# Kernel tuning notes

Measured on AMD Instinct MI355X. Metric: run time of the kernel, lower is better.

## Reference

```python
import jax, jax.numpy as jnp
import numpy as np

# Dimensions derived from Mamba.__init__: d_model=512 -> joint_latent=32, mamb_latent=D=640
NL, D, DIN, DS, DTR, DC = 4, 640, 1280, 16, 40, 4  # n_layer, d_model, d_inner, d_state, dt_rank, d_conv
B, V = 64, 30  # batch, joint-sequence length (repeat_joint_num)


def _rms(x, w, eps=1e-5):
    return x * jax.lax.rsqrt(jnp.mean(x * x, axis=-1, keepdims=True) + eps) * w


def _mamba_block(x, in_w, conv_w, conv_b, xp_w, dt_w, dt_b, A_log, D_skip, out_w):
    # x: [B, V, D]
    u, res = jnp.split(jnp.einsum('bvd,ed->bve', x, in_w), 2, axis=-1)  # each [B,V,DIN]
    # causal depthwise conv1d over V
    xc = jnp.pad(u.transpose(0, 2, 1), ((0, 0), (0, 0), (DC - 1, 0)))  # [B,DIN,V+DC-1]
    xc = jax.lax.conv_general_dilated(xc, conv_w[:, None, :], (1,), 'VALID',
                                      feature_group_count=DIN,
                                      dimension_numbers=('NCH', 'OIH', 'NCH'))
    u = jax.nn.silu(xc.transpose(0, 2, 1) + conv_b)  # [B,V,DIN]
    # input-dependent SSM params
    dbl = jnp.einsum('bvd,ed->bve', u, xp_w)  # [B,V,DTR+2*DS]
    delta, Bm, Cm = jnp.split(dbl, [DTR, DTR + DS], axis=-1)
    delta = jax.nn.softplus(jnp.einsum('bvr,dr->bvd', delta, dt_w) + dt_b)  # [B,V,DIN]
    A = -jnp.exp(A_log)  # [DIN,DS]
    dA = jnp.exp(delta[..., None] * A)                              # [B,V,DIN,DS]
    dBu = delta[..., None] * Bm[:, :, None, :] * u[..., None]       # [B,V,DIN,DS]

    def step(h, t):
        dA_t, dBu_t, C_t = t
        h = dA_t * h + dBu_t                      # [B,DIN,DS]
        return h, jnp.einsum('bds,bs->bd', h, C_t)

    h0 = jnp.zeros((x.shape[0], DIN, DS), x.dtype)
    _, ys = jax.lax.scan(step, h0, (dA.transpose(1, 0, 2, 3),
                                    dBu.transpose(1, 0, 2, 3),
                                    Cm.transpose(1, 0, 2)))
    y = ys.transpose(1, 0, 2) + u * D_skip        # [B,V,DIN]
    return jnp.einsum('bvd,ed->bve', y * jax.nn.silu(res), out_w)


def setup_inputs() -> dict:
    key = jax.random.key(0)
    ks = jax.random.split(key, 10)
    s = 0.02
    return {
        'x': jax.random.normal(ks[0], (B, V, D), jnp.float32),
        'vs': jax.random.randint(ks[1], (B,), 0, V),
        'norm_w': jnp.ones((NL, D), jnp.float32),
        'in_proj_w': s * jax.random.normal(ks[2], (NL, 2 * DIN, D), jnp.float32),
        'conv_w': s * jax.random.normal(ks[3], (NL, DIN, DC), jnp.float32),
        'conv_b': jnp.zeros((NL, DIN), jnp.float32),
        'x_proj_w': s * jax.random.normal(ks[4], (NL, DTR + 2 * DS, DIN), jnp.float32),
        'dt_proj_w': s * jax.random.normal(ks[5], (NL, DIN, DTR), jnp.float32),
        'dt_proj_b': jnp.full((NL, DIN), -4.0, jnp.float32) + 0.1 * jax.random.normal(ks[6], (NL, DIN), jnp.float32),
        'A_log': jnp.tile(jnp.log(jnp.arange(1.0, DS + 1.0, dtype=jnp.float32)), (NL, DIN, 1)),
        'D_skip': jnp.ones((NL, DIN), jnp.float32),
        'out_proj_w': s * jax.random.normal(ks[7], (NL, D, DIN), jnp.float32),
        'norm_f_w': jnp.ones((D,), jnp.float32),
    }


def reference(x, vs, norm_w, in_proj_w, conv_w, conv_b, x_proj_w, dt_proj_w,
              dt_proj_b, A_log, D_skip, out_proj_w, norm_f_w):
    bidx = jnp.arange(x.shape[0])[:, None]
    # batch-wise circular permutation over V (circular_permute_v)
    fwd_idx = (jnp.arange(V)[None, :] + V - vs[:, None]) % V  # [B,V]
    h = x[bidx, fwd_idx]
    for i in range(NL):
        h = h + _mamba_block(_rms(h, norm_w[i]), in_proj_w[i], conv_w[i], conv_b[i],
                             x_proj_w[i], dt_proj_w[i], dt_proj_b[i], A_log[i],
                             D_skip[i], out_proj_w[i])
    h = _rms(h, norm_f_w)
    # reverse_circular_permute_v
    rev_idx = (jnp.arange(V)[None, :] + vs[:, None]) % V
    return h[bidx, rev_idx]
```

## Files before the change

### kernel.cpp

```cpp
#include <hip/hip_runtime.h>
#include <math.h>

#define NLAYER 4
#define DMODEL 640
#define DINNER 1280
#define DSTATE 16
#define DTRANK 40
#define DCONV  4
#define BATCH  64
#define SEQ    30
#define MTOK   (BATCH*SEQ)
#define NPROJ  (2*DINNER)
#define NDBL   (DTRANK+2*DSTATE)
#define NDBLP  80
#define KSEGS  8
#define KSEG   (DINNER/KSEGS)
#define DTKP   64

#define Q1 (NLAYER*NPROJ*DMODEL/4)
#define Q2 (NLAYER*DMODEL*DINNER/4)
#define Q3 (NLAYER*NDBLP*DINNER/4)
#define Q4 (NLAYER*DINNER*DTKP/4)
#define WCTOT (Q1+Q2+Q3+Q4)

typedef unsigned short u16;
typedef __bf16 bf16x8 __attribute__((ext_vector_type(8)));
typedef float  f32x4  __attribute__((ext_vector_type(4)));
typedef unsigned short u16x8 __attribute__((ext_vector_type(8)));

__device__ __forceinline__ float siluf(float x) {
    return x / (1.0f + __expf(-x));
}

__device__ __forceinline__ u16 f2bf(float f) {
    unsigned int u = __float_as_uint(f);
    u += 0x7fffu + ((u >> 16) & 1u);
    return (u16)(u >> 16);
}

__device__ __forceinline__ float bf2f(u16 b) {
    return __uint_as_float(((unsigned int)b) << 16);
}

__global__ void k_permute(const float* __restrict__ x, const int* __restrict__ vs,
                          float* __restrict__ h) {
    int idx = blockIdx.x * blockDim.x + threadIdx.x;
    if (idx >= MTOK * DMODEL) return;
    int d  = idx % DMODEL;
    int mv = idx / DMODEL;
    int v  = mv % SEQ;
    int b  = mv / SEQ;
    int src = (v + SEQ - vs[b]) % SEQ;
    h[idx] = x[(b * SEQ + src) * DMODEL + d];
}

__global__ __launch_bounds__(256)
void k_wconv(const float* __restrict__ in_w, const float* __restrict__ out_w,
             const float* __restrict__ xp_w, const float* __restrict__ dt_w,
             u16* __restrict__ wbi, u16* __restrict__ wbo,
             u16* __restrict__ wbx, u16* __restrict__ wdt) {
    int i = blockIdx.x * 256 + threadIdx.x;
    if (i < Q1) {
        int j = i * 4;
        float4 v = *(const float4*)(in_w + j);
        ushort4 o;
        o.x = f2bf(v.x); o.y = f2bf(v.y); o.z = f2bf(v.z); o.w = f2bf(v.w);
        *(ushort4*)(wbi + j) = o;
    } else if (i < Q1 + Q2) {
        int j = (i - Q1) * 4;
        float4 v = *(const float4*)(out_w + j);
        ushort4 o;
        o.x = f2bf(v.x); o.y = f2bf(v.y); o.z = f2bf(v.z); o.w = f2bf(v.w);
        *(ushort4*)(wbo + j) = o;
    } else if (i < Q1 + Q2 + Q3) {
        int j = (i - Q1 - Q2) * 4;
        int layer = j / (NDBLP * DINNER);
        int rem   = j % (NDBLP * DINNER);
        int r = rem / DINNER, c = rem % DINNER;
        ushort4 o = make_ushort4(0, 0, 0, 0);
        if (r < NDBL) {
            float4 v = *(const float4*)(xp_w + ((size_t)layer * NDBL + r) * DINNER + c);
            o.x = f2bf(v.x); o.y = f2bf(v.y); o.z = f2bf(v.z); o.w = f2bf(v.w);
        }
        *(ushort4*)(wbx + j) = o;
    } else {
        int j = (i - Q1 - Q2 - Q3) * 4;
        int ld = j / DTKP;
        int c  = j % DTKP;
        ushort4 o = make_ushort4(0, 0, 0, 0);
        if (c < DTRANK) {
            float4 v = *(const float4*)(dt_w + (size_t)ld * DTRANK + c);
            o.x = f2bf(v.x); o.y = f2bf(v.y); o.z = f2bf(v.z); o.w = f2bf(v.w);
        }
        *(ushort4*)(wdt + j) = o;
    }
}

__global__ __launch_bounds__(64)
void k_rmsnorm(const float* __restrict__ h, const float* __restrict__ w,
               u16* __restrict__ xn) {
    int m = blockIdx.x;
    int t = threadIdx.x;
    const float* row = h + (size_t)m * DMODEL;
    float2 vv[5];
    float ss = 0.f;
    #pragma unroll
    for (int i = 0; i < 5; ++i) {
        vv[i] = *(const float2*)(row + i * 128 + t * 2);
        ss += vv[i].x * vv[i].x + vv[i].y * vv[i].y;
    }
    #pragma unroll
    for (int o = 32; o > 0; o >>= 1) ss += __shfl_xor(ss, o, 64);
    float sc = rsqrtf(ss / DMODEL + 1e-5f);
    u16* outp = xn + (size_t)m * DMODEL;
    #pragma unroll
    for (int i = 0; i < 5; ++i) {
        int d = i * 128 + t * 2;
        float2 wv = *(const float2*)(w + d);
        ushort2 o;
        o.x = f2bf(vv[i].x * sc * wv.x);
        o.y = f2bf(vv[i].y * sc * wv.y);
        *(ushort2*)(outp + d) = o;
    }
}

__global__ __launch_bounds__(512)
void k_mfma512(const u16* __restrict__ A, int lda,
               const u16* __restrict__ W,
               u16* __restrict__ Cb, int N, int K) {
    __shared__ u16 As[2][128 * 64];
    __shared__ u16 Bs[2][128 * 64];
    const int t = threadIdx.x;
    const int w = t >> 6, l = t & 63;
    const int lane15 = l & 15, quad = l >> 4;
    const int wm = w >> 1, wn = w & 1;
    const int m0 = blockIdx.y * 128, n0 = blockIdx.x * 128;

    f32x4 acc[2][4];
    #pragma unroll
    for (int i = 0; i < 2; ++i)
        #pragma unroll
        for (int j = 0; j < 4; ++j)
            acc[i][j] = (f32x4){0.f, 0.f, 0.f, 0.f};

    auto stage = [&](int buf, int k0) {
        #pragma unroll
        for (int q = 0; q < 2; ++q) {
            int c   = q * 512 + t;
            int row = c >> 3;
            int gch = ((c & 7) ^ (row & 7)) * 8;
            const u16* ga = A + (size_t)(m0 + row) * lda + k0 + gch;
            __builtin_amdgcn_global_load_lds(
                (const __attribute__((address_space(1))) void*)ga,
                (__attribute__((address_space(3))) void*)&As[buf][c * 8], 16, 0, 0);
            const u16* gb = W + (size_t)(n0 + row) * K + k0 + gch;
            __builtin_amdgcn_global_load_lds(
                (const __attribute__((address_space(1))) void*)gb,
                (__attribute__((address_space(3))) void*)&Bs[buf][c * 8], 16, 0, 0);
        }
    };

    auto compute = [&](int buf) {
        #pragma unroll
        for (int ks = 0; ks < 2; ++ks) {
            bf16x8 af[2], bfr[4];
            #pragma unroll
            for (int i = 0; i < 2; ++i) {
                int row = wm * 32 + i * 16 + lane15;
                af[i] = *(const bf16x8*)&As[buf][row * 64 + (((ks * 4 + quad) ^ (row & 7)) * 8)];
            }
            #pragma unroll
            for (int j = 0; j < 4; ++j) {
                int row = wn * 64 + j * 16 + lane15;
                bfr[j] = *(const bf16x8*)&Bs[buf][row * 64 + (((ks * 4 + quad) ^ (row & 7)) * 8)];
            }
            #pragma unroll
            for (int i = 0; i < 2; ++i)
                #pragma unroll
                for (int j = 0; j < 4; ++j)
                    acc[i][j] = __builtin_amdgcn_mfma_f32_16x16x32_bf16(
                        af[i], bfr[j], acc[i][j], 0, 0, 0);
        }
    };

    const int NT = K >> 6;
    stage(0, 0);
    __syncthreads();
    int cur = 0;
    for (int tt = 1; tt < NT; ++tt) {
        stage(cur ^ 1, tt * 64);
        compute(cur);
        __syncthreads();
        cur ^= 1;
    }
    compute(cur);

    #pragma unroll
    for (int i = 0; i < 2; ++i) {
        #pragma unroll
        for (int r = 0; r < 4; ++r) {
            int row = m0 + wm * 32 + i * 16 + quad * 4 + r;
            #pragma unroll
            for (int j = 0; j < 4; ++j) {
                int col = n0 + wn * 64 + j * 16 + lane15;
                Cb[(size_t)row * N + col] = f2bf(acc[i][j][r]);
            }
        }
    }
}

__global__ __launch_bounds__(256)
void k_mfma64(const u16* __restrict__ A, int lda,
              const u16* __restrict__ W,
              const float* __restrict__ resid,
              float* __restrict__ C, int N, int K) {
    __shared__ u16 As[2][64 * 64];
    __shared__ u16 Bs[2][64 * 64];
    const int t = threadIdx.x;
    const int w = t >> 6, l = t & 63;
    const int lane15 = l & 15, quad = l >> 4;
    const int wm = w >> 1, wn = w & 1;
    const int m0 = blockIdx.y * 64, n0 = blockIdx.x * 64;

    f32x4 acc[2][2];
    #pragma unroll
    for (int i = 0; i < 2; ++i)
        #pragma unroll
        for (int j = 0; j < 2; ++j)
            acc[i][j] = (f32x4){0.f, 0.f, 0.f, 0.f};

    auto stage = [&](int buf, int k0) {
        #pragma unroll
        for (int q = 0; q < 2; ++q) {
            int c   = q * 256 + t;
            int row = c >> 3;
            int gch = ((c & 7) ^ (row & 7)) * 8;
            const u16* ga = A + (size_t)(m0 + row) * lda + k0 + gch;
            __builtin_amdgcn_global_load_lds(
                (const __attribute__((address_space(1))) void*)ga,
                (__attribute__((address_space(3))) void*)&As[buf][c * 8], 16, 0, 0);
            const u16* gb = W + (size_t)(n0 + row) * K + k0 + gch;
            __builtin_amdgcn_global_load_lds(
                (const __attribute__((address_space(1))) void*)gb,
                (__attribute__((address_space(3))) void*)&Bs[buf][c * 8], 16, 0, 0);
        }
    };

    auto compute = [&](int buf) {
        #pragma unroll
        for (int ks = 0; ks < 2; ++ks) {
            bf16x8 af[2], bfr[2];
            #pragma unroll
            for (int i = 0; i < 2; ++i) {
                int row = wm * 32 + i * 16 + lane15;
                af[i] = *(const bf16x8*)&As[buf][row * 64 + (((ks * 4 + quad) ^ (row & 7)) * 8)];
            }
            #pragma unroll
            for (int j = 0; j < 2; ++j) {
                int row = wn * 32 + j * 16 + lane15;
                bfr[j] = *(const bf16x8*)&Bs[buf][row * 64 + (((ks * 4 + quad) ^ (row & 7)) * 8)];
            }
            #pragma unroll
            for (int i = 0; i < 2; ++i)
                #pragma unroll
                for (int j = 0; j < 2; ++j)
                    acc[i][j] = __builtin_amdgcn_mfma_f32_16x16x32_bf16(
                        af[i], bfr[j], acc[i][j], 0, 0, 0);
        }
    };

    const int NT = K >> 6;
    stage(0, 0);
    __syncthreads();
    int cur = 0;
    for (int tt = 1; tt < NT; ++tt) {
        stage(cur ^ 1, tt * 64);
        compute(cur);
        __syncthreads();
        cur ^= 1;
    }
    compute(cur);

    #pragma unroll
    for (int i = 0; i < 2; ++i) {
        #pragma unroll
        for (int r = 0; r < 4; ++r) {
            int row = m0 + wm * 32 + i * 16 + quad * 4 + r;
            #pragma unroll
            for (int j = 0; j < 2; ++j) {
                int col = n0 + wn * 32 + j * 16 + lane15;
                size_t idx = (size_t)row * N + col;
                float v = acc[i][j][r];
                if (resid) v += resid[idx];
                C[idx] = v;
            }
        }
    }
}

__global__ __launch_bounds__(256)
void k_conv(const u16* __restrict__ urb, const float* __restrict__ cw,
            const float* __restrict__ cb, u16* __restrict__ ubf) {
    int idx = blockIdx.x * 256 + threadIdx.x;
    int c = idx % DINNER;
    int b = idx / DINNER;
    const u16* up = urb + (size_t)(b * SEQ) * NPROJ + c;
    float xv[SEQ];
    #pragma unroll
    for (int v = 0; v < SEQ; ++v) xv[v] = bf2f(up[(size_t)v * NPROJ]);
    float w0 = cw[c * 4 + 0], w1 = cw[c * 4 + 1];
    float w2 = cw[c * 4 + 2], w3 = cw[c * 4 + 3];
    float bias = cb[c];
    u16* op = ubf + (size_t)(b * SEQ) * DINNER + c;
    float x0 = 0.f, x1 = 0.f, x2 = 0.f;
    #pragma unroll
    for (int v = 0; v < SEQ; ++v) {
        float x3 = xv[v];
        float o = bias + w0 * x0 + w1 * x1 + w2 * x2 + w3 * x3;
        op[(size_t)v * DINNER] = f2bf(siluf(o));
        x0 = x1; x1 = x2; x2 = x3;
    }
}

__global__ __launch_bounds__(256)
void k_xproj(const u16* __restrict__ ubf, const u16* __restrict__ wbx,
             float* __restrict__ dblp) {
    __shared__ u16 As[64 * 32];
    __shared__ u16 Bs[NDBLP * 32];
    const int t = threadIdx.x;
    const int w = t >> 6, l = t & 63;
    const int lane15 = l & 15, quad = l >> 4;
    const int seg = blockIdx.x;
    const int m0 = blockIdx.y * 64;
    const int kb = seg * KSEG;

    f32x4 acc[5];
    #pragma unroll
    for (int j = 0; j < 5; ++j) acc[j] = (f32x4){0.f, 0.f, 0.f, 0.f};

    for (int k0 = 0; k0 < KSEG; k0 += 32) {
        __syncthreads();
        {
            int c = t;
            const u16* ga = ubf + (size_t)(m0 + (c >> 2)) * DINNER + kb + k0 + (c & 3) * 8;
            __builtin_amdgcn_global_load_lds(
                (const __attribute__((address_space(1))) void*)ga,
                (__attribute__((address_space(3))) void*)&As[c * 8], 16, 0, 0);
            const u16* gb = wbx + (size_t)(c >> 2) * DINNER + kb + k0 + (c & 3) * 8;
            __builtin_amdgcn_global_load_lds(
                (const __attribute__((address_space(1))) void*)gb,
                (__attribute__((address_space(3))) void*)&Bs[c * 8], 16, 0, 0);
        }
        if (t < 64) {
            int c = 256 + t;
            const u16* gb = wbx + (size_t)(c >> 2) * DINNER + kb + k0 + (c & 3) * 8;
            __builtin_amdgcn_global_load_lds(
                (const __attribute__((address_space(1))) void*)gb,
                (__attribute__((address_space(3))) void*)&Bs[c * 8], 16, 0, 0);
        }
        __syncthreads();

        bf16x8 af = *(const bf16x8*)&As[(w * 16 + lane15) * 32 + quad * 8];
        #pragma unroll
        for (int j = 0; j < 5; ++j) {
            bf16x8 bfrag = *(const bf16x8*)&Bs[(j * 16 + lane15) * 32 + quad * 8];
            acc[j] = __builtin_amdgcn_mfma_f32_16x16x32_bf16(af, bfrag, acc[j], 0, 0, 0);
        }
    }

    float* outp = dblp + (size_t)seg * MTOK * NDBLP;
    #pragma unroll
    for (int r = 0; r < 4; ++r) {
        int row = m0 + w * 16 + quad * 4 + r;
        #pragma unroll
        for (int j = 0; j < 5; ++j) {
            int col = j * 16 + lane15;
            outp[(size_t)row * NDBLP + col] = acc[j][r];
        }
    }
}

__global__ __launch_bounds__(256)
void k_dtgemm(const float* __restrict__ dblp, const u16* __restrict__ dtwb,
              const float* __restrict__ dtb, u16* __restrict__ delta) {
    __shared__ u16 As[64 * 32];
    __shared__ u16 Bs[64 * 32];
    const int t = threadIdx.x;
    const int w = t >> 6, l = t & 63;
    const int lane15 = l & 15, quad = l >> 4;
    const int wm = w >> 1, wn = w & 1;
    const int m0 = blockIdx.y * 64, n0 = blockIdx.x * 64;
    const int row = t >> 2, koff = (t & 3) * 8;
    const int m = m0 + row;

    f32x4 acc[2][2];
    #pragma unroll
    for (int i = 0; i < 2; ++i)
        #pragma unroll
        for (int j = 0; j < 2; ++j)
            acc[i][j] = (f32x4){0.f, 0.f, 0.f, 0.f};

    #pragma unroll
    for (int k0 = 0; k0 < DTKP; k0 += 32) {
        float sums[8] = {0.f, 0.f, 0.f, 0.f, 0.f, 0.f, 0.f, 0.f};
        #pragma unroll
        for (int q = 0; q < 2; ++q) {
            int col = k0 + koff + q * 4;
            if (col < DTRANK) {
                #pragma unroll
                for (int sg = 0; sg < KSEGS; ++sg) {
                    float4 p = *(const float4*)&dblp[(size_t)sg * MTOK * NDBLP
                                                     + (size_t)m * NDBLP + col];
                    sums[q * 4 + 0] += p.x; sums[q * 4 + 1] += p.y;
                    sums[q * 4 + 2] += p.z; sums[q * 4 + 3] += p.w;
                }
            }
        }
        u16x8 av;
        #pragma unroll
        for (int e = 0; e < 8; ++e) av[e] = f2bf(sums[e]);
        __syncthreads();
        *(u16x8*)&As[row * 32 + koff] = av;
        {
            int c = t;
            const u16* gb = dtwb + (size_t)(n0 + (c >> 2)) * DTKP + k0 + (c & 3) * 8;
            __builtin_amdgcn_global_load_lds(
                (const __attribute__((address_space(1))) void*)gb,
                (__attribute__((address_space(3))) void*)&Bs[c * 8], 16, 0, 0);
        }
        __syncthreads();

        bf16x8 af[2], bfrag[2];
        #pragma unroll
        for (int i = 0; i < 2; ++i)
            af[i] = *(const bf16x8*)&As[(wm * 32 + i * 16 + lane15) * 32 + quad * 8];
        #pragma unroll
        for (int j = 0; j < 2; ++j)
            bfrag[j] = *(const bf16x8*)&Bs[(wn * 32 + j * 16 + lane15) * 32 + quad * 8];
        #pragma unroll
        for (int i = 0; i < 2; ++i)
            #pragma unroll
            for (int j = 0; j < 2; ++j)
                acc[i][j] = __builtin_amdgcn_mfma_f32_16x16x32_bf16(
                    af[i], bfrag[j], acc[i][j], 0, 0, 0);
    }

    #pragma unroll
    for (int i = 0; i < 2; ++i) {
        #pragma unroll
        for (int r = 0; r < 4; ++r) {
            int orow = m0 + wm * 32 + i * 16 + quad * 4 + r;
            #pragma unroll
            for (int j = 0; j < 2; ++j) {
                int col = n0 + wn * 32 + j * 16 + lane15;
                float vv = acc[i][j][r] + dtb[col];
                vv = (vv > 20.f) ? vv : log1pf(__expf(vv));
                delta[(size_t)orow * DINNER + col] = f2bf(vv);
            }
        }
    }
}

__global__ __launch_bounds__(256)
void k_scan(const u16* __restrict__ ubf, const u16* __restrict__ urb,
            const float* __restrict__ dblp, const u16* __restrict__ delta,
            const float* __restrict__ A_log, const float* __restrict__ Dsk,
            u16* __restrict__ y) {
    __shared__ float BC[SEQ][2 * DSTATE];
    const int b  = blockIdx.x / (DINNER / 256);
    const int dc = blockIdx.x % (DINNER / 256);
    const int d  = dc * 256 + threadIdx.x;

    for (int t = threadIdx.x; t < SEQ * 2 * DSTATE; t += 256) {
        int v = t >> 5, s = t & 31;
        float acc = 0.f;
        #pragma unroll
        for (int sg = 0; sg < KSEGS; ++sg)
            acc += dblp[(size_t)sg * MTOK * NDBLP + (size_t)(b * SEQ + v) * NDBLP + DTRANK + s];
        BC[v][s] = acc;
    }
    __syncthreads();

    float dl[SEQ], uu[SEQ], rr[SEQ];
    #pragma unroll
    for (int v = 0; v < SEQ; ++v)
        dl[v] = bf2f(delta[(size_t)(b * SEQ + v) * DINNER + d]);
    #pragma unroll
    for (int v = 0; v < SEQ; ++v)
        uu[v] = bf2f(ubf[(size_t)(b * SEQ + v) * DINNER + d]);
    #pragma unroll
    for (int v = 0; v < SEQ; ++v)
        rr[v] = bf2f(urb[(size_t)(b * SEQ + v) * NPROJ + DINNER + d]);

    float Ar[DSTATE];
    #pragma unroll
    for (int s = 0; s < DSTATE; ++s) Ar[s] = -__expf(A_log[(size_t)d * DSTATE + s]);
    float dsk = Dsk[d];
    float st[DSTATE];
    #pragma unroll
    for (int s = 0; s < DSTATE; ++s) st[s] = 0.f;

    u16* yp = y + (size_t)(b * SEQ) * DINNER + d;

    #pragma unroll
    for (int v = 0; v < SEQ; ++v) {
        float dlt = dl[v];
        float du  = dlt * uu[v];
        float ya0 = 0.f, ya1 = 0.f, ya2 = 0.f, ya3 = 0.f;
        #pragma unroll
        for (int s = 0; s < DSTATE; s += 4) {
            float dA0 = __expf(dlt * Ar[s + 0]);
            float dA1 = __expf(dlt * Ar[s + 1]);
            float dA2 = __expf(dlt * Ar[s + 2]);
            float dA3 = __expf(dlt * Ar[s + 3]);
            st[s + 0] = dA0 * st[s + 0] + du * BC[v][s + 0];
            st[s + 1] = dA1 * st[s + 1] + du * BC[v][s + 1];
            st[s + 2] = dA2 * st[s + 2] + du * BC[v][s + 2];
            st[s + 3] = dA3 * st[s + 3] + du * BC[v][s + 3];
            ya0 += st[s + 0] * BC[v][DSTATE + s + 0];
            ya1 += st[s + 1] * BC[v][DSTATE + s + 1];
            ya2 += st[s + 2] * BC[v][DSTATE + s + 2];
            ya3 += st[s + 3] * BC[v][DSTATE + s + 3];
        }
        float ya = (ya0 + ya1) + (ya2 + ya3);
        yp[(size_t)v * DINNER] = f2bf((ya + uu[v] * dsk) * siluf(rr[v]));
    }
}

__global__ __launch_bounds__(64)
void k_final(const float* __restrict__ h, const int* __restrict__ vs,
             const float* __restrict__ w, float* __restrict__ out) {
    int mv = blockIdx.x;
    int v = mv % SEQ, b = mv / SEQ;
    int src = (v + vs[b]) % SEQ;
    const float* row = h + (size_t)(b * SEQ + src) * DMODEL;
    int t = threadIdx.x;
    float ss = 0.f;
    for (int d = t; d < DMODEL; d += 64) { float x = row[d]; ss += x * x; }
    #pragma unroll
    for (int o = 32; o > 0; o >>= 1) ss += __shfl_xor(ss, o, 64);
    float sc = rsqrtf(ss / DMODEL + 1e-5f);
    float* op = out + (size_t)mv * DMODEL;
    for (int d = t; d < DMODEL; d += 64) op[d] = row[d] * sc * w[d];
}

extern "C" void kernel_launch(void* const* d_in, const int* in_sizes, int n_in,
                              void* d_out, int out_size, void* d_ws, size_t ws_size,
                              hipStream_t stream) {
    const float* x      = (const float*)d_in[0];
    const int*   vs     = (const int*)d_in[1];
    const float* norm_w = (const float*)d_in[2];
    const float* in_w   = (const float*)d_in[3];
    const float* conv_w = (const float*)d_in[4];
    const float* conv_b = (const float*)d_in[5];
    const float* xp_w   = (const float*)d_in[6];
    const float* dt_w   = (const float*)d_in[7];
    const float* dt_b   = (const float*)d_in[8];
    const float* A_log  = (const float*)d_in[9];
    const float* Dsk    = (const float*)d_in[10];
    const float* out_w  = (const float*)d_in[11];
    const float* nfw    = (const float*)d_in[12];
    float* out = (float*)d_out;

    char* p = (char*)d_ws;
    float* h      = (float*)p; p += (size_t)MTOK * DMODEL * 4;
    u16*   xn     = (u16*)p;   p += (size_t)MTOK * DMODEL * 2;
    u16*   urb    = (u16*)p;   p += (size_t)MTOK * NPROJ * 2;
    u16*   ubf    = (u16*)p;   p += (size_t)MTOK * DINNER * 2;
    float* dblp   = (float*)p; p += (size_t)KSEGS * MTOK * NDBLP * 4;
    u16*   deltab = (u16*)p;   p += (size_t)MTOK * DINNER * 2;
    u16*   y      = (u16*)p;   p += (size_t)MTOK * DINNER * 2;
    u16*   wbi4   = (u16*)p;   p += (size_t)NLAYER * NPROJ * DMODEL * 2;
    u16*   wbo4   = (u16*)p;   p += (size_t)NLAYER * DMODEL * DINNER * 2;
    u16*   wbx4   = (u16*)p;   p += (size_t)NLAYER * NDBLP * DINNER * 2;
    u16*   wdt4   = (u16*)p;   p += (size_t)NLAYER * DINNER * DTKP * 2;

    k_wconv<<<WCTOT / 256, 256, 0, stream>>>(
        in_w, out_w, xp_w, dt_w, wbi4, wbo4, wbx4, wdt4);

    k_permute<<<(MTOK * DMODEL + 255) / 256, 256, 0, stream>>>(x, vs, h);

    for (int l = 0; l < NLAYER; ++l) {
        k_rmsnorm<<<MTOK, 64, 0, stream>>>(h, norm_w + (size_t)l * DMODEL, xn);

        k_mfma512<<<dim3(NPROJ / 128, MTOK / 128), 512, 0, stream>>>(
            xn, DMODEL, wbi4 + (size_t)l * NPROJ * DMODEL, urb, NPROJ, DMODEL);

        k_conv<<<BATCH * DINNER / 256, 256, 0, stream>>>(
            urb, conv_w + (size_t)l * DINNER * DCONV, conv_b + (size_t)l * DINNER, ubf);

        k_xproj<<<dim3(KSEGS, MTOK / 64), 256, 0, stream>>>(
            ubf, wbx4 + (size_t)l * NDBLP * DINNER, dblp);

        k_dtgemm<<<dim3(DINNER / 64, MTOK / 64), 256, 0, stream>>>(
            dblp, wdt4 + (size_t)l * DINNER * DTKP,
            dt_b + (size_t)l * DINNER, deltab);

        k_scan<<<BATCH * (DINNER / 256), 256, 0, stream>>>(
            ubf, urb, dblp, deltab,
            A_log + (size_t)l * DINNER * DSTATE, Dsk + (size_t)l * DINNER, y);

        k_mfma64<<<dim3(DMODEL / 64, MTOK / 64), 256, 0, stream>>>(
            y, DINNER, wbo4 + (size_t)l * DMODEL * DINNER, h, h, DMODEL, DINNER);
    }

    k_final<<<MTOK, 64, 0, stream>>>(h, vs, nfw, out);
}
```

Measured before the change: 466.3 us.

## Fuse rmsnorm into in-proj, conv into x-proj, and dt-proj into scan

Merges three producer/consumer kernel pairs per layer: the RMSNorm is computed inside the in-projection GEMM prologue, the causal conv+SiLU is computed directly into LDS for the x-projection, and the dt-projection with softplus feeds the selective scan through shared memory. The scan also splits the 16 state dims across two lanes, combining them with a shuffle. This removes the xn and delta intermediate buffers and cuts launches from six to three per layer before the out-projection. In exchange, A is no longer double-buffered in the in-proj GEMM (an extra barrier per k-step), the conv recomputes reads with strided loads, and the dt-proj tile uses 60-row blocks with clamped rows.

New measurement: 692.2 us. 48.5% more time.

```diff
diff --git a/kernel.cpp b/kernel.cpp
--- a/kernel.cpp
+++ b/kernel.cpp
@@ -96,46 +96,37 @@
     }
 }
 
-__global__ __launch_bounds__(64)
-void k_rmsnorm(const float* __restrict__ h, const float* __restrict__ w,
-               u16* __restrict__ xn) {
-    int m = blockIdx.x;
-    int t = threadIdx.x;
-    const float* row = h + (size_t)m * DMODEL;
-    float2 vv[5];
-    float ss = 0.f;
-    #pragma unroll
-    for (int i = 0; i < 5; ++i) {
-        vv[i] = *(const float2*)(row + i * 128 + t * 2);
-        ss += vv[i].x * vv[i].x + vv[i].y * vv[i].y;
-    }
-    #pragma unroll
-    for (int o = 32; o > 0; o >>= 1) ss += __shfl_xor(ss, o, 64);
-    float sc = rsqrtf(ss / DMODEL + 1e-5f);
-    u16* outp = xn + (size_t)m * DMODEL;
-    #pragma unroll
-    for (int i = 0; i < 5; ++i) {
-        int d = i * 128 + t * 2;
-        float2 wv = *(const float2*)(w + d);
-        ushort2 o;
-        o.x = f2bf(vv[i].x * sc * wv.x);
-        o.y = f2bf(vv[i].y * sc * wv.y);
-        *(ushort2*)(outp + d) = o;
-    }
-}
-
 __global__ __launch_bounds__(512)
-void k_mfma512(const u16* __restrict__ A, int lda,
-               const u16* __restrict__ W,
-               u16* __restrict__ Cb, int N, int K) {
-    __shared__ u16 As[2][128 * 64];
+void k_norm_inproj(const float* __restrict__ h, const float* __restrict__ nw,
+                   const u16* __restrict__ W, u16* __restrict__ Cb) {
+    __shared__ u16 As[128 * 72];
     __shared__ u16 Bs[2][128 * 64];
+    __shared__ float scale[128];
     const int t = threadIdx.x;
     const int w = t >> 6, l = t & 63;
     const int lane15 = l & 15, quad = l >> 4;
     const int wm = w >> 1, wn = w & 1;
     const int m0 = blockIdx.y * 128, n0 = blockIdx.x * 128;
 
+    {
+        int row = t >> 2, part = t & 3;
+        const float* hp = h + (size_t)(m0 + row) * DMODEL + part * 160;
+        float ss = 0.f;
+        #pragma unroll
+        for (int i = 0; i < 40; ++i) {
+            float4 v = *(const float4*)(hp + i * 4);
+            ss += v.x * v.x + v.y * v.y + v.z * v.z + v.w * v.w;
+        }
+        ((float*)As)[row * 4 + part] = ss;
+    }
+    __syncthreads();
+    if (t < 128) {
+        const float* ps = (const float*)As;
+        float s = ps[t * 4] + ps[t * 4 + 1] + ps[t * 4 + 2] + ps[t * 4 + 3];
+        scale[t] = rsqrtf(s / DMODEL + 1e-5f);
+    }
+    __syncthreads();
+
     f32x4 acc[2][4];
     #pragma unroll
     for (int i = 0; i < 2; ++i)
@@ -143,32 +134,48 @@
         for (int j = 0; j < 4; ++j)
             acc[i][j] = (f32x4){0.f, 0.f, 0.f, 0.f};
 
-    auto stage = [&](int buf, int k0) {
+    auto stageB = [&](int buf, int k0) {
         #pragma unroll
         for (int q = 0; q < 2; ++q) {
             int c   = q * 512 + t;
             int row = c >> 3;
             int gch = ((c & 7) ^ (row & 7)) * 8;
-            const u16* ga = A + (size_t)(m0 + row) * lda + k0 + gch;
-            __builtin_amdgcn_global_load_lds(
-                (const __attribute__((address_space(1))) void*)ga,
-                (__attribute__((address_space(3))) void*)&As[buf][c * 8], 16, 0, 0);
-            const u16* gb = W + (size_t)(n0 + row) * K + k0 + gch;
+            const u16* gb = W + (size_t)(n0 + row) * DMODEL + k0 + gch;
             __builtin_amdgcn_global_load_lds(
                 (const __attribute__((address_space(1))) void*)gb,
                 (__attribute__((address_space(3))) void*)&Bs[buf][c * 8], 16, 0, 0);
         }
     };
 
+    auto stageA = [&](int k0) {
+        #pragma unroll
+        for (int q = 0; q < 2; ++q) {
+            int row = q * 64 + (t >> 3);
+            int ch  = t & 7;
+            const float* hp = h + (size_t)(m0 + row) * DMODEL + k0 + ch * 8;
+            float4 a0 = *(const float4*)hp;
+            float4 a1 = *(const float4*)(hp + 4);
+            const float* wp = nw + k0 + ch * 8;
+            float4 w0 = *(const float4*)wp;
+            float4 w1 = *(const float4*)(wp + 4);
+            float sc = scale[row];
+            u16x8 o;
+            o[0] = f2bf(a0.x * sc * w0.x); o[1] = f2bf(a0.y * sc * w0.y);
+            o[2] = f2bf(a0.z * sc * w0.z); o[3] = f2bf(a0.w * sc * w0.w);
+            o[4] = f2bf(a1.x * sc * w1.x); o[5] = f2bf(a1.y * sc * w1.y);
+            o[6] = f2bf(a1.z * sc * w1.z); o[7] = f2bf(a1.w * sc * w1.w);
+            *(u16x8*)&As[row * 72 + ch * 8] = o;
+        }
+    };
+
     auto compute = [&](int buf) {
         #pragma unroll
         for (int ks = 0; ks < 2; ++ks) {
             bf16x8 af[2], bfr[4];
             #pragma unroll
-            for (int i = 0; i < 2; ++i) {
-                int row = wm * 32 + i * 16 + lane15;
-                af[i] = *(const bf16x8*)&As[buf][row * 64 + (((ks * 4 + quad) ^ (row & 7)) * 8)];
-            }
+            for (int i = 0; i < 2; ++i)
+                af[i] = *(const bf16x8*)&As[(wm * 32 + i * 16 + lane15) * 72
+                                            + (ks * 4 + quad) * 8];
             #pragma unroll
             for (int j = 0; j < 4; ++j) {
                 int row = wn * 64 + j * 16 + lane15;
@@ -183,14 +190,17 @@
         }
     };
 
-    const int NT = K >> 6;
-    stage(0, 0);
+    const int NT = DMODEL / 64;
+    stageB(0, 0);
+    stageA(0);
     __syncthreads();
     int cur = 0;
     for (int tt = 1; tt < NT; ++tt) {
-        stage(cur ^ 1, tt * 64);
+        stageB(cur ^ 1, tt * 64);
         compute(cur);
         __syncthreads();
+        stageA(tt * 64);
+        __syncthreads();
         cur ^= 1;
     }
     compute(cur);
@@ -203,7 +213,7 @@
             #pragma unroll
             for (int j = 0; j < 4; ++j) {
                 int col = n0 + wn * 64 + j * 16 + lane15;
-                Cb[(size_t)row * N + col] = f2bf(acc[i][j][r]);
+                Cb[(size_t)row * NPROJ + col] = f2bf(acc[i][j][r]);
             }
         }
     }
@@ -299,34 +309,11 @@
 }
 
 __global__ __launch_bounds__(256)
-void k_conv(const u16* __restrict__ urb, const float* __restrict__ cw,
-            const float* __restrict__ cb, u16* __restrict__ ubf) {
-    int idx = blockIdx.x * 256 + threadIdx.x;
-    int c = idx % DINNER;
-    int b = idx / DINNER;
-    const u16* up = urb + (size_t)(b * SEQ) * NPROJ + c;
-    float xv[SEQ];
-    #pragma unroll
-    for (int v = 0; v < SEQ; ++v) xv[v] = bf2f(up[(size_t)v * NPROJ]);
-    float w0 = cw[c * 4 + 0], w1 = cw[c * 4 + 1];
-    float w2 = cw[c * 4 + 2], w3 = cw[c * 4 + 3];
-    float bias = cb[c];
-    u16* op = ubf + (size_t)(b * SEQ) * DINNER + c;
-    float x0 = 0.f, x1 = 0.f, x2 = 0.f;
-    #pragma unroll
-    for (int v = 0; v < SEQ; ++v) {
-        float x3 = xv[v];
-        float o = bias + w0 * x0 + w1 * x1 + w2 * x2 + w3 * x3;
-        op[(size_t)v * DINNER] = f2bf(siluf(o));
-        x0 = x1; x1 = x2; x2 = x3;
-    }
-}
-
-__global__ __launch_bounds__(256)
-void k_xproj(const u16* __restrict__ ubf, const u16* __restrict__ wbx,
-             float* __restrict__ dblp) {
-    __shared__ u16 As[64 * 32];
-    __shared__ u16 Bs[NDBLP * 32];
+void k_convxproj(const u16* __restrict__ urb, const float* __restrict__ cw,
+                 const float* __restrict__ cb, const u16* __restrict__ wbx,
+                 u16* __restrict__ ubf, float* __restrict__ dblp) {
+    __shared__ u16 Au[64 * 168];
+    __shared__ u16 Bsx[80 * 168];
     const int t = threadIdx.x;
     const int w = t >> 6, l = t & 63;
     const int lane15 = l & 15, quad = l >> 4;
@@ -334,36 +321,38 @@
     const int m0 = blockIdx.y * 64;
     const int kb = seg * KSEG;
 
+    for (int o = t; o < 64 * KSEG; o += 256) {
+        int row = o / KSEG, cc = o - row * KSEG;
+        int token = m0 + row;
+        int b = token / SEQ, v = token - b * SEQ;
+        int c = kb + cc;
+        float4 wv = *(const float4*)(cw + c * 4);
+        float accv = cb[c];
+        if (v >= 1) accv += wv.z * bf2f(urb[(size_t)(b * SEQ + v - 1) * NPROJ + c]);
+        if (v >= 2) accv += wv.y * bf2f(urb[(size_t)(b * SEQ + v - 2) * NPROJ + c]);
+        if (v >= 3) accv += wv.x * bf2f(urb[(size_t)(b * SEQ + v - 3) * NPROJ + c]);
+        accv += wv.w * bf2f(urb[(size_t)(b * SEQ + v) * NPROJ + c]);
+        u16 bv = f2bf(siluf(accv));
+        Au[row * 168 + cc] = bv;
+        ubf[(size_t)token * DINNER + c] = bv;
+    }
+    for (int o = t; o < 80 * (KSEG / 8); o += 256) {
+        int row = o / 20, ch = o - row * 20;
+        u16x8 vv = *(const u16x8*)(wbx + (size_t)row * DINNER + kb + ch * 8);
+        *(u16x8*)&Bsx[row * 168 + ch * 8] = vv;
+    }
+    __syncthreads();
+
     f32x4 acc[5];
     #pragma unroll
     for (int j = 0; j < 5; ++j) acc[j] = (f32x4){0.f, 0.f, 0.f, 0.f};
 
+    #pragma unroll
     for (int k0 = 0; k0 < KSEG; k0 += 32) {
-        __syncthreads();
-        {
-            int c = t;
-            const u16* ga = ubf + (size_t)(m0 + (c >> 2)) * DINNER + kb + k0 + (c & 3) * 8;
-            __builtin_amdgcn_global_load_lds(
-                (const __attribute__((address_space(1))) void*)ga,
-                (__attribute__((address_space(3))) void*)&As[c * 8], 16, 0, 0);
-            const u16* gb = wbx + (size_t)(c >> 2) * DINNER + kb + k0 + (c & 3) * 8;
-            __builtin_amdgcn_global_load_lds(
-                (const __attribute__((address_space(1))) void*)gb,
-                (__attribute__((address_space(3))) void*)&Bs[c * 8], 16, 0, 0);
-        }
-        if (t < 64) {
-            int c = 256 + t;
-            const u16* gb = wbx + (size_t)(c >> 2) * DINNER + kb + k0 + (c & 3) * 8;
-            __builtin_amdgcn_global_load_lds(
-                (const __attribute__((address_space(1))) void*)gb,
-                (__attribute__((address_space(3))) void*)&Bs[c * 8], 16, 0, 0);
-        }
-        __syncthreads();
-
-        bf16x8 af = *(const bf16x8*)&As[(w * 16 + lane15) * 32 + quad * 8];
+        bf16x8 af = *(const bf16x8*)&Au[(w * 16 + lane15) * 168 + k0 + quad * 8];
         #pragma unroll
         for (int j = 0; j < 5; ++j) {
-            bf16x8 bfrag = *(const bf16x8*)&Bs[(j * 16 + lane15) * 32 + quad * 8];
+            bf16x8 bfrag = *(const bf16x8*)&Bsx[(j * 16 + lane15) * 168 + k0 + quad * 8];
             acc[j] = __builtin_amdgcn_mfma_f32_16x16x32_bf16(af, bfrag, acc[j], 0, 0, 0);
         }
     }
@@ -381,17 +370,35 @@
 }
 
 __global__ __launch_bounds__(256)
-void k_dtgemm(const float* __restrict__ dblp, const u16* __restrict__ dtwb,
-              const float* __restrict__ dtb, u16* __restrict__ delta) {
+void k_dtscan(const float* __restrict__ dblp, const u16* __restrict__ dtwb,
+              const float* __restrict__ dtb,
+              const u16* __restrict__ ubf, const u16* __restrict__ urb,
+              const float* __restrict__ A_log, const float* __restrict__ Dsk,
+              u16* __restrict__ y) {
     __shared__ u16 As[64 * 32];
     __shared__ u16 Bs[64 * 32];
+    __shared__ float ldelta[64][64];
+    __shared__ float BC2[2][SEQ][32];
     const int t = threadIdx.x;
     const int w = t >> 6, l = t & 63;
     const int lane15 = l & 15, quad = l >> 4;
     const int wm = w >> 1, wn = w & 1;
-    const int m0 = blockIdx.y * 64, n0 = blockIdx.x * 64;
+    const int n0 = blockIdx.x * 64;
+    const int m0 = blockIdx.y * 60;
     const int row = t >> 2, koff = (t & 3) * 8;
-    const int m = m0 + row;
+    const int mm = min(m0 + row, MTOK - 1);
+
+    for (int s0 = t; s0 < 2 * SEQ * 32; s0 += 256) {
+        int lb  = s0 / (SEQ * 32);
+        int rem = s0 - lb * SEQ * 32;
+        int v = rem >> 5, st = rem & 31;
+        int token = m0 + lb * SEQ + v;
+        float a = 0.f;
+        #pragma unroll
+        for (int sg = 0; sg < KSEGS; ++sg)
+            a += dblp[(size_t)sg * MTOK * NDBLP + (size_t)token * NDBLP + DTRANK + st];
+        BC2[lb][v][st] = a;
+    }
 
     f32x4 acc[2][2];
     #pragma unroll
@@ -410,7 +417,7 @@
                 #pragma unroll
                 for (int sg = 0; sg < KSEGS; ++sg) {
                     float4 p = *(const float4*)&dblp[(size_t)sg * MTOK * NDBLP
-                                                     + (size_t)m * NDBLP + col];
+                                                     + (size_t)mm * NDBLP + col];
                     sums[q * 4 + 0] += p.x; sums[q * 4 + 1] += p.y;
                     sums[q * 4 + 2] += p.z; sums[q * 4 + 3] += p.w;
                 }
@@ -449,42 +456,25 @@
     for (int i = 0; i < 2; ++i) {
         #pragma unroll
         for (int r = 0; r < 4; ++r) {
-            int orow = m0 + wm * 32 + i * 16 + quad * 4 + r;
+            int orow = wm * 32 + i * 16 + quad * 4 + r;
             #pragma unroll
             for (int j = 0; j < 2; ++j) {
-                int col = n0 + wn * 32 + j * 16 + lane15;
-                float vv = acc[i][j][r] + dtb[col];
+                int col = wn * 32 + j * 16 + lane15;
+                float vv = acc[i][j][r] + dtb[n0 + col];
                 vv = (vv > 20.f) ? vv : log1pf(__expf(vv));
-                delta[(size_t)orow * DINNER + col] = f2bf(vv);
-            }
-        }
-    }
-}
-
-__global__ __launch_bounds__(256)
-void k_scan(const u16* __restrict__ ubf, const u16* __restrict__ urb,
-            const float* __restrict__ dblp, const u16* __restrict__ delta,
-            const float* __restrict__ A_log, const float* __restrict__ Dsk,
-            u16* __restrict__ y) {
-    __shared__ float BC[SEQ][2 * DSTATE];
-    const int b  = blockIdx.x / (DINNER / 256);
-    const int dc = blockIdx.x % (DINNER / 256);
-    const int d  = dc * 256 + threadIdx.x;
-
-    for (int t = threadIdx.x; t < SEQ * 2 * DSTATE; t += 256) {
-        int v = t >> 5, s = t & 31;
-        float acc = 0.f;
-        #pragma unroll
-        for (int sg = 0; sg < KSEGS; ++sg)
-            acc += dblp[(size_t)sg * MTOK * NDBLP + (size_t)(b * SEQ + v) * NDBLP + DTRANK + s];
-        BC[v][s] = acc;
+                ldelta[orow][col] = vv;
+            }
+        }
     }
     __syncthreads();
 
-    float dl[SEQ], uu[SEQ], rr[SEQ];
-    #pragma unroll
-    for (int v = 0; v < SEQ; ++v)
-        dl[v] = bf2f(delta[(size_t)(b * SEQ + v) * DINNER + d]);
+    const int lb   = t >> 7;
+    const int dloc = (t >> 1) & 63;
+    const int half = t & 1;
+    const int d    = n0 + dloc;
+    const int b    = m0 / SEQ + lb;
+
+    float uu[SEQ], rr[SEQ];
     #pragma unroll
     for (int v = 0; v < SEQ; ++v)
         uu[v] = bf2f(ubf[(size_t)(b * SEQ + v) * DINNER + d]);
@@ -492,38 +482,41 @@
     for (int v = 0; v < SEQ; ++v)
         rr[v] = bf2f(urb[(size_t)(b * SEQ + v) * NPROJ + DINNER + d]);
 
-    float Ar[DSTATE];
-    #pragma unroll
-    for (int s = 0; s < DSTATE; ++s) Ar[s] = -__expf(A_log[(size_t)d * DSTATE + s]);
+    float Ar[8];
+    #pragma unroll
+    for (int s = 0; s < 8; ++s)
+        Ar[s] = -__expf(A_log[(size_t)d * DSTATE + half * 8 + s]);
     float dsk = Dsk[d];
-    float st[DSTATE];
-    #pragma unroll
-    for (int s = 0; s < DSTATE; ++s) st[s] = 0.f;
+    float st8[8];
+    #pragma unroll
+    for (int s = 0; s < 8; ++s) st8[s] = 0.f;
 
     u16* yp = y + (size_t)(b * SEQ) * DINNER + d;
 
     #pragma unroll
     for (int v = 0; v < SEQ; ++v) {
-        float dlt = dl[v];
+        float dlt = ldelta[lb * SEQ + v][dloc];
         float du  = dlt * uu[v];
-        float ya0 = 0.f, ya1 = 0.f, ya2 = 0.f, ya3 = 0.f;
-        #pragma unroll
-        for (int s = 0; s < DSTATE; s += 4) {
+        float ya = 0.f, yb = 0.f;
+        #pragma unroll
+        for (int s = 0; s < 8; s += 4) {
             float dA0 = __expf(dlt * Ar[s + 0]);
             float dA1 = __expf(dlt * Ar[s + 1]);
             float dA2 = __expf(dlt * Ar[s + 2]);
             float dA3 = __expf(dlt * Ar[s + 3]);
-            st[s + 0] = dA0 * st[s + 0] + du * BC[v][s + 0];
-            st[s + 1] = dA1 * st[s + 1] + du * BC[v][s + 1];
-            st[s + 2] = dA2 * st[s + 2] + du * BC[v][s + 2];
-            st[s + 3] = dA3 * st[s + 3] + du * BC[v][s + 3];
-            ya0 += st[s + 0] * BC[v][DSTATE + s + 0];
-            ya1 += st[s + 1] * BC[v][DSTATE + s + 1];
-            ya2 += st[s + 2] * BC[v][DSTATE + s + 2];
-            ya3 += st[s + 3] * BC[v][DSTATE + s + 3];
-        }
-        float ya = (ya0 + ya1) + (ya2 + ya3);
-        yp[(size_t)v * DINNER] = f2bf((ya + uu[v] * dsk) * siluf(rr[v]));
+            st8[s + 0] = dA0 * st8[s + 0] + du * BC2[lb][v][half * 8 + s + 0];
+            st8[s + 1] = dA1 * st8[s + 1] + du * BC2[lb][v][half * 8 + s + 1];
+            st8[s + 2] = dA2 * st8[s + 2] + du * BC2[lb][v][half * 8 + s + 2];
+            st8[s + 3] = dA3 * st8[s + 3] + du * BC2[lb][v][half * 8 + s + 3];
+            ya += st8[s + 0] * BC2[lb][v][DSTATE + half * 8 + s + 0];
+            yb += st8[s + 1] * BC2[lb][v][DSTATE + half * 8 + s + 1];
+            ya += st8[s + 2] * BC2[lb][v][DSTATE + half * 8 + s + 2];
+            yb += st8[s + 3] * BC2[lb][v][DSTATE + half * 8 + s + 3];
+        }
+        float yh = ya + yb;
+        yh += __shfl_xor(yh, 1, 64);
+        if (half == 0)
+            yp[(size_t)v * DINNER] = f2bf((yh + uu[v] * dsk) * siluf(rr[v]));
     }
 }
 
@@ -564,11 +557,9 @@
 
     char* p = (char*)d_ws;
     float* h      = (float*)p; p += (size_t)MTOK * DMODEL * 4;
-    u16*   xn     = (u16*)p;   p += (size_t)MTOK * DMODEL * 2;
     u16*   urb    = (u16*)p;   p += (size_t)MTOK * NPROJ * 2;
     u16*   ubf    = (u16*)p;   p += (size_t)MTOK * DINNER * 2;
     float* dblp   = (float*)p; p += (size_t)KSEGS * MTOK * NDBLP * 4;
-    u16*   deltab = (u16*)p;   p += (size_t)MTOK * DINNER * 2;
     u16*   y      = (u16*)p;   p += (size_t)MTOK * DINNER * 2;
     u16*   wbi4   = (u16*)p;   p += (size_t)NLAYER * NPROJ * DMODEL * 2;
     u16*   wbo4   = (u16*)p;   p += (size_t)NLAYER * DMODEL * DINNER * 2;
@@ -581,24 +572,16 @@
     k_permute<<<(MTOK * DMODEL + 255) / 256, 256, 0, stream>>>(x, vs, h);
 
     for (int l = 0; l < NLAYER; ++l) {
-        k_rmsnorm<<<MTOK, 64, 0, stream>>>(h, norm_w + (size_t)l * DMODEL, xn);
-
-        k_mfma512<<<dim3(NPROJ / 128, MTOK / 128), 512, 0, stream>>>(
-            xn, DMODEL, wbi4 + (size_t)l * NPROJ * DMODEL, urb, NPROJ, DMODEL);
-
-        k_conv<<<BATCH * DINNER / 256, 256, 0, stream>>>(
-            urb, conv_w + (size_t)l * DINNER * DCONV, conv_b + (size_t)l * DINNER, ubf);
-
-        k_xproj<<<dim3(KSEGS, MTOK / 64), 256, 0, stream>>>(
-            ubf, wbx4 + (size_t)l * NDBLP * DINNER, dblp);
-
-        k_dtgemm<<<dim3(DINNER / 64, MTOK / 64), 256, 0, stream>>>(
-            dblp, wdt4 + (size_t)l * DINNER * DTKP,
-            dt_b + (size_t)l * DINNER, deltab);
-
-        k_scan<<<BATCH * (DINNER / 256), 256, 0, stream>>>(
-            ubf, urb, dblp, deltab,
-            A_log + (size_t)l * DINNER * DSTATE, Dsk + (size_t)l * DINNER, y);
+        k_norm_inproj<<<dim3(NPROJ / 128, MTOK / 128), 512, 0, stream>>>(
+            h, norm_w + (size_t)l * DMODEL, wbi4 + (size_t)l * NPROJ * DMODEL, urb);
+
+        k_convxproj<<<dim3(KSEGS, MTOK / 64), 256, 0, stream>>>(
+            urb, conv_w + (size_t)l * DINNER * DCONV, conv_b + (size_t)l * DINNER,
+            wbx4 + (size_t)l * NDBLP * DINNER, ubf, dblp);
+
+        k_dtscan<<<dim3(DINNER / 64, MTOK / 60), 256, 0, stream>>>(
+            dblp, wdt4 + (size_t)l * DINNER * DTKP, dt_b + (size_t)l * DINNER,
+            ubf, urb, A_log + (size_t)l * DINNER * DSTATE, Dsk + (size_t)l * DINNER, y);
 
         k_mfma64<<<dim3(DMODEL / 64, MTOK / 64), 256, 0, stream>>>(
             y, DINNER, wbo4 + (size_t)l * DMODEL * DINNER, h, h, DMODEL, DINNER);
```
